# Performance work log

Measured on AMD Instinct MI355X. Metric: run time of the kernel, lower is better.

Reference implementation:

```python
import math
import jax, jax.numpy as jnp
import numpy as np

LOW_FREQ = 1
FACTOR = 1


def setup_inputs() -> dict:
    key = jax.random.key(0)
    x = jax.random.normal(key, (16, 4096, 256), dtype=jnp.float32)
    return {"x": x}


def reference(x):
    b, t, d = x.shape
    x_freq = jnp.fft.rfft(x, axis=1)  # (b, t//2+1, d) complex
    if t % 2 == 0:
        x_freq = x_freq[:, LOW_FREQ:-1]
        f = jnp.fft.rfftfreq(t)[LOW_FREQ:-1]
    else:
        x_freq = x_freq[:, LOW_FREQ:]
        f = jnp.fft.rfftfreq(t)[LOW_FREQ:]
    f = f.astype(jnp.float32)
    F = x_freq.shape[1]
    top_k = int(FACTOR * math.log(F))  # static (shape-derived)

    # top-k by magnitude along freq axis, independently per (b, d)
    xf_bdf = jnp.moveaxis(x_freq, 1, 2)              # (b, d, F)
    _, idx = jax.lax.top_k(jnp.abs(xf_bdf), top_k)   # (b, d, k) int32
    xf_sel = jnp.take_along_axis(xf_bdf, idx, axis=2)  # (b, d, k)
    xf_sel = jnp.moveaxis(xf_sel, 2, 1)              # (b, k, d)
    f_sel = jnp.moveaxis(f[idx], 2, 1)[:, :, None, :]  # (b, k, 1, d)

    # extrapolate: conj-pair frequencies, synthesize cosines, reduce over freq
    xf2 = jnp.concatenate([xf_sel, jnp.conj(xf_sel)], axis=1)  # (b, 2k, d)
    f2 = jnp.concatenate([f_sel, -f_sel], axis=1)              # (b, 2k, 1, d)
    tt = jnp.arange(t, dtype=jnp.float32)[None, None, :, None]  # (1,1,t,1)
    amp = (jnp.abs(xf2) * 2.0 / t)[:, :, None, :]   # (b, 2k, 1, d)
    phase = jnp.angle(xf2)[:, :, None, :]           # (b, 2k, 1, d)
    x_time = amp * jnp.cos(2.0 * math.pi * f2 * tt + phase)  # (b, 2k, t, d)
    return x_time.sum(axis=1)  # (b, t, d)
```

## Files before the change

kernel.cpp:

```cpp
#include <hip/hip_runtime.h>
#include <math.h>

#define T_LEN 4096
#define N2    2048
#define TOPK  7
#define NCH   256
#define R8F 0.70710678f

#define AD(a) ((a) + ((a) >> 3) + ((a) >> 8))

__global__ __launch_bounds__(256) void prep_kernel(
    const float* __restrict__ x, float* __restrict__ xt,
    double2* __restrict__ tw, float2* __restrict__ twf)
{
    if (blockIdx.x < 16) {
        int p = blockIdx.x * 256 + threadIdx.x;
        double th = -2.0 * 3.14159265358979323846 * (double)p / (double)T_LEN;
        double c = cos(th), s = sin(th);
        tw[p]  = make_double2(c, s);
        twf[p] = make_float2((float)c, (float)s);
        return;
    }
    __shared__ float tile[64][65];
    const int bid = blockIdx.x - 16;
    const int t0  = (bid & 63) * 64;
    const int c0  = ((bid >> 6) & 3) * 64;
    const int b   = bid >> 8;
    const int tx4 = (threadIdx.x & 15) * 4;
    const int ty  = threadIdx.x >> 4;

    const float* src = x + (size_t)b * T_LEN * NCH;
    for (int r = 0; r < 4; ++r) {
        int t = ty + r * 16;
        float4 v = *(const float4*)(src + (size_t)(t0 + t) * NCH + c0 + tx4);
        tile[t][tx4 + 0] = v.x; tile[t][tx4 + 1] = v.y;
        tile[t][tx4 + 2] = v.z; tile[t][tx4 + 3] = v.w;
    }
    __syncthreads();
    float* dst = xt + (size_t)b * NCH * T_LEN;
    for (int r = 0; r < 4; ++r) {
        int c = ty + r * 16;
        float4 v = make_float4(tile[tx4 + 0][c], tile[tx4 + 1][c],
                               tile[tx4 + 2][c], tile[tx4 + 3][c]);
        *(float4*)(dst + (size_t)(c0 + c) * T_LEN + t0 + tx4) = v;
    }
}

__device__ __forceinline__ void dft8_twf(float ar[8], float ai[8],
                                         int base, const float2* __restrict__ twf)
{
    float t0r=ar[0]+ar[4], t0i=ai[0]+ai[4], t4r=ar[0]-ar[4], t4i=ai[0]-ai[4];
    float t1r=ar[1]+ar[5], t1i=ai[1]+ai[5], t5r=ar[1]-ar[5], t5i=ai[1]-ai[5];
    float t2r=ar[2]+ar[6], t2i=ai[2]+ai[6], t6r=ar[2]-ar[6], t6i=ai[2]-ai[6];
    float t3r=ar[3]+ar[7], t3i=ai[3]+ai[7], t7r=ar[3]-ar[7], t7i=ai[3]-ai[7];
    float s0r=t0r+t2r, s0i=t0i+t2i, s2r=t0r-t2r, s2i=t0i-t2i;
    float s1r=t1r+t3r, s1i=t1i+t3i, s3r=t1r-t3r, s3i=t1i-t3i;
    ar[0]=s0r+s1r; ai[0]=s0i+s1i;
    ar[4]=s0r-s1r; ai[4]=s0i-s1i;
    ar[2]=s2r+s3i; ai[2]=s2i-s3r;
    ar[6]=s2r-s3i; ai[6]=s2i+s3r;
    float c1r=R8F*(t5r+t5i), c1i=R8F*(t5i-t5r);
    float c2r=t6i,           c2i=-t6r;
    float c3r=R8F*(t7i-t7r), c3i=-R8F*(t7r+t7i);
    float d0r=t4r+c2r, d0i=t4i+c2i, d1r=t4r-c2r, d1i=t4i-c2i;
    float d2r=c1r+c3r, d2i=c1i+c3i, d3r=c1r-c3r, d3i=c1i-c3i;
    ar[1]=d0r+d2r; ai[1]=d0i+d2i;
    ar[5]=d0r-d2r; ai[5]=d0i-d2i;
    ar[3]=d1r+d3i; ai[3]=d1i-d3r;
    ar[7]=d1r-d3i; ai[7]=d1i+d3r;
#pragma unroll
    for (int m = 1; m < 8; ++m) {
        float2 w = twf[(base * m) & 4095];
        float xr = ar[m], xi = ai[m];
        ar[m] = w.x * xr - w.y * xi;
        ai[m] = w.x * xi + w.y * xr;
    }
}

__device__ __forceinline__ unsigned long long packkey32(float mag, int k) {
    return ((unsigned long long)__float_as_uint(mag) << 32)
         | (unsigned long long)(2047 - k);
}

__global__ __launch_bounds__(256, 8) void fft_topk_kernel(
    const float* __restrict__ xt, const double2* __restrict__ tw,
    const float2* __restrict__ twf,
    int* __restrict__ k_out, float4* __restrict__ ab4)
{
    __shared__ float2 zz[AD(N2 - 1) + 3];
    __shared__ unsigned long long wavetop[4 * TOPK];
    __shared__ unsigned long long selkey[TOPK];

    const int tid = threadIdx.x;
    const int bc  = blockIdx.x;
    const float2* xcol2 = (const float2*)(xt + (size_t)bc * T_LEN);

    float ar[8], ai[8];
#pragma unroll
    for (int u = 0; u < 8; ++u) {
        float2 v = xcol2[tid + (u << 8)];
        ar[u] = v.x; ai[u] = v.y;
    }
    dft8_twf(ar, ai, 2 * tid, twf);
#pragma unroll
    for (int m = 0; m < 8; ++m)
        zz[AD((m << 8) + tid)] = make_float2(ar[m], ai[m]);
    __syncthreads();

    {
        const int g = tid >> 5, j2 = tid & 31, base = (g << 8) + j2;
#pragma unroll
        for (int u = 0; u < 8; ++u) {
            float2 v = zz[AD(base + (u << 5))];
            ar[u] = v.x; ai[u] = v.y;
        }
        dft8_twf(ar, ai, 16 * j2, twf);
#pragma unroll
        for (int m = 0; m < 8; ++m)
            zz[AD(base + (m << 5))] = make_float2(ar[m], ai[m]);
    }
    __syncthreads();

    {
        const int g3 = tid >> 2, j3 = tid & 3, base = (g3 << 5) + j3;
#pragma unroll
        for (int u = 0; u < 8; ++u) {
            float2 v = zz[AD(base + (u << 2))];
            ar[u] = v.x; ai[u] = v.y;
        }
        dft8_twf(ar, ai, 128 * j3, twf);
#pragma unroll
        for (int m = 0; m < 8; ++m)
            zz[AD(base + (m << 2))] = make_float2(ar[m], ai[m]);
    }
    __syncthreads();

#pragma unroll
    for (int q = 0; q < 2; ++q) {
        int h4 = ((q << 8) + tid) << 2;
#pragma unroll
        for (int r = 0; r < 4; ++r) {
            float2 v = zz[AD(h4 + r)];
            ar[q * 4 + r] = v.x; ai[q * 4 + r] = v.y;
        }
    }
    __syncthreads();
#pragma unroll
    for (int q = 0; q < 2; ++q) {
        float b0r = ar[q*4+0], b0i = ai[q*4+0], b1r = ar[q*4+1], b1i = ai[q*4+1];
        float b2r = ar[q*4+2], b2i = ai[q*4+2], b3r = ar[q*4+3], b3i = ai[q*4+3];
        float e0r = b0r + b2r, e0i = b0i + b2i, e1r = b0r - b2r, e1i = b0i - b2i;
        float e2r = b1r + b3r, e2i = b1i + b3i, e3r = b1r - b3r, e3i = b1i - b3i;
        int kbase = ((tid & 7) << 6) | (((tid >> 3) & 7) << 3) | (q << 2) | (tid >> 6);
        zz[AD(kbase)]        = make_float2(e0r + e2r, e0i + e2i);
        zz[AD(kbase + 1024)] = make_float2(e0r - e2r, e0i - e2i);
        zz[AD(kbase +  512)] = make_float2(e1r + e3i, e1i - e3r);
        zz[AD(kbase + 1536)] = make_float2(e1r - e3i, e1i + e3r);
    }
    __syncthreads();

    unsigned long long keys[8];
#pragma unroll
    for (int j = 0; j < 4; ++j) {
        int k  = 1 + tid + (j << 8);
        int kp = N2 - k;
        float2 yk = zz[AD(k)];
        float2 yp = zz[AD(kp)];
        float Ar = 0.5f * (yk.x + yp.x), Ai = 0.5f * (yk.y - yp.y);
        float Br = 0.5f * (yk.y + yp.y), Bi = -0.5f * (yk.x - yp.x);
        float2 t = twf[k];
        float Cr = t.x * Br - t.y * Bi;
        float Ci = t.x * Bi + t.y * Br;
        float m1 = (Ar + Cr) * (Ar + Cr) + (Ai + Ci) * (Ai + Ci);
        float m2 = (Ar - Cr) * (Ar - Cr) + (Ai - Ci) * (Ai - Ci);
        keys[2 * j]     = packkey32(m1, k);
        keys[2 * j + 1] = (kp != k) ? packkey32(m2, kp) : 0ULL;
    }

    const int wv = tid >> 6, ln = tid & 63;
    unsigned long long lb = 0ULL;
#pragma unroll
    for (int s = 0; s < 8; ++s) lb = (keys[s] > lb) ? keys[s] : lb;

    for (int it = 0; it < TOPK; ++it) {
        unsigned long long v = lb;
#pragma unroll
        for (int off = 32; off; off >>= 1) {
            unsigned long long o = __shfl_xor(v, off);
            if (o > v) v = o;
        }
        if (ln == 0) wavetop[wv * TOPK + it] = v;
#pragma unroll
        for (int s = 0; s < 8; ++s) keys[s] = (keys[s] == v) ? 0ULL : keys[s];
        lb = 0ULL;
#pragma unroll
        for (int s = 0; s < 8; ++s) lb = (keys[s] > lb) ? keys[s] : lb;
    }
    __syncthreads();

    if (tid < 32) {
        unsigned long long v = (tid < 4 * TOPK) ? wavetop[tid] : 0ULL;
        for (int it = 0; it < TOPK; ++it) {
            unsigned long long m = v;
#pragma unroll
            for (int off = 16; off; off >>= 1) {
                unsigned long long o = __shfl_xor(m, off);
                if (o > m) m = o;
            }
            if (tid == 0) selkey[it] = m;
            if (m == v) v = 0ULL;
        }
    }
    __syncthreads();

    if (tid < TOPK) {
        int k  = 2047 - (int)(selkey[tid] & 2047ULL);
        float2 ykf = zz[AD(k)];
        float2 ypf = zz[AD(N2 - k)];
        double ykx = (double)ykf.x, yky = (double)ykf.y;
        double ypx = (double)ypf.x, ypy = (double)ypf.y;
        double Ar = 0.5 * (ykx + ypx), Ai = 0.5 * (yky - ypy);
        double Br = 0.5 * (yky + ypy), Bi = -0.5 * (ykx - ypx);
        double2 t = tw[k];
        double Xr = Ar + t.x * Br - t.y * Bi;
        double Xi = Ai + t.x * Bi + t.y * Br;
        k_out[tid * 4096 + bc] = k;
        ab4[tid * 4096 + bc] = make_float4(
            (float)( 4.0 * Xr / (double)T_LEN),
            (float)(-4.0 * Xi / (double)T_LEN),
            (float)t.x, (float)(-t.y));
    }
}

__global__ __launch_bounds__(256) void recon_kernel(
    const int* __restrict__ k_in, const float4* __restrict__ ab4,
    float* __restrict__ out)
{
    __shared__ float tile[16][256];

    const int tid   = threadIdx.x;
    const int chunk = blockIdx.x & 127;
    const int b     = blockIdx.x >> 7;
    const int bc    = (b << 8) + tid;
    const int n0    = chunk << 5;

    const float c0 = 6.28318530717958647692f / 4096.0f;
    float aa[TOPK], bb[TOPK], zr[TOPK], zi[TOPK], wr[TOPK], wi[TOPK];
#pragma unroll
    for (int j = 0; j < TOPK; ++j) {
        int k    = k_in[j * 4096 + bc];
        float4 v = ab4[j * 4096 + bc];
        aa[j] = v.x; bb[j] = v.y; wr[j] = v.z; wi[j] = v.w;
        int m0 = (k * n0) & (T_LEN - 1);
        float ang = (float)m0 * c0;
        zr[j] = __cosf(ang);
        zi[j] = __sinf(ang);
    }

    float* obase = out + ((size_t)b * T_LEN + n0) * NCH;
    for (int r = 0; r < 2; ++r) {
#pragma unroll
        for (int i = 0; i < 16; ++i) {
            float acc = 0.f;
#pragma unroll
            for (int j = 0; j < TOPK; ++j) {
                acc += aa[j] * zr[j] + bb[j] * zi[j];
                float nzr = zr[j] * wr[j] - zi[j] * wi[j];
                zi[j] = zr[j] * wi[j] + zi[j] * wr[j];
                zr[j] = nzr;
            }
            tile[i][tid] = acc;
        }
        __syncthreads();
#pragma unroll
        for (int s = 0; s < 4; ++s) {
            int fid = tid + (s << 8);
            int ni  = fid >> 6;
            int c4  = (fid & 63) << 2;
            float4 v = make_float4(tile[ni][c4], tile[ni][c4 + 1],
                                   tile[ni][c4 + 2], tile[ni][c4 + 3]);
            *(float4*)(obase + (size_t)((r << 4) + ni) * NCH + c4) = v;
        }
        __syncthreads();
    }
}

extern "C" void kernel_launch(void* const* d_in, const int* in_sizes, int n_in,
                              void* d_out, int out_size, void* d_ws, size_t ws_size,
                              hipStream_t stream) {
    const float* x   = (const float*)d_in[0];
    float*       out = (float*)d_out;
    char*        ws  = (char*)d_ws;

    double2* tw    = (double2*)(ws);
    int*     k_ws  = (int*)   (ws + 65536);
    float4*  ab_ws = (float4*)(ws + 180224);
    float2*  twf   = (float2*)(ws + 638976);

    prep_kernel     <<<16 + 4096, 256, 0, stream>>>(x, out, tw, twf);
    fft_topk_kernel <<<4096, 256, 0, stream>>>(out, tw, twf, k_ws, ab_ws);
    recon_kernel    <<<2048, 256, 0, stream>>>(k_ws, ab_ws, out);
}
```

Measured before the change: 186.8 us.

## Compute FFT twiddles by powers, sort keys for top-k, halve recon blocks

Each radix-8 stage now loads one twiddle and builds its powers in registers instead of making seven table loads. Per-thread keys are sorted once with a sorting network, so each top-k round only shifts the list instead of rescanning all eight keys. The reconstruction kernel covers 64 time steps per block with half as many blocks, and re-seeds the recurrence with sincos every 16 steps to limit error build-up. The trade-offs are slightly lower twiddle accuracy from the power chain and fewer blocks in flight in recon.

```diff
diff --git a/kernel.cpp b/kernel.cpp
--- a/kernel.cpp
+++ b/kernel.cpp
@@ -46,8 +46,14 @@
     }
 }
 
-__device__ __forceinline__ void dft8_twf(float ar[8], float ai[8],
-                                         int base, const float2* __restrict__ twf)
+__device__ __forceinline__ void cmulf(float& xr, float& xi, float wrr, float wii) {
+    float r = wrr * xr - wii * xi;
+    xi = wrr * xi + wii * xr;
+    xr = r;
+}
+
+__device__ __forceinline__ void dft8_pw(float ar[8], float ai[8],
+                                        float w1r, float w1i)
 {
     float t0r=ar[0]+ar[4], t0i=ai[0]+ai[4], t4r=ar[0]-ar[4], t4i=ai[0]-ai[4];
     float t1r=ar[1]+ar[5], t1i=ai[1]+ai[5], t5r=ar[1]-ar[5], t5i=ai[1]-ai[5];
@@ -68,19 +74,29 @@
     ar[5]=d0r-d2r; ai[5]=d0i-d2i;
     ar[3]=d1r+d3i; ai[3]=d1i-d3r;
     ar[7]=d1r-d3i; ai[7]=d1i+d3r;
-#pragma unroll
-    for (int m = 1; m < 8; ++m) {
-        float2 w = twf[(base * m) & 4095];
-        float xr = ar[m], xi = ai[m];
-        ar[m] = w.x * xr - w.y * xi;
-        ai[m] = w.x * xi + w.y * xr;
-    }
+
+    float w2r = w1r*w1r - w1i*w1i, w2i = 2.0f*w1r*w1i;
+    float w3r = w2r*w1r - w2i*w1i, w3i = w2r*w1i + w2i*w1r;
+    float w4r = w2r*w2r - w2i*w2i, w4i = 2.0f*w2r*w2i;
+    float w5r = w3r*w2r - w3i*w2i, w5i = w3r*w2i + w3i*w2r;
+    float w6r = w3r*w3r - w3i*w3i, w6i = 2.0f*w3r*w3i;
+    float w7r = w4r*w3r - w4i*w3i, w7i = w4r*w3i + w4i*w3r;
+    cmulf(ar[1], ai[1], w1r, w1i);
+    cmulf(ar[2], ai[2], w2r, w2i);
+    cmulf(ar[3], ai[3], w3r, w3i);
+    cmulf(ar[4], ai[4], w4r, w4i);
+    cmulf(ar[5], ai[5], w5r, w5i);
+    cmulf(ar[6], ai[6], w6r, w6i);
+    cmulf(ar[7], ai[7], w7r, w7i);
 }
 
 __device__ __forceinline__ unsigned long long packkey32(float mag, int k) {
     return ((unsigned long long)__float_as_uint(mag) << 32)
          | (unsigned long long)(2047 - k);
 }
+
+#define CSWAP(i, j) { unsigned long long a_ = keys[i], b_ = keys[j]; \
+                      keys[i] = a_ > b_ ? a_ : b_; keys[j] = a_ > b_ ? b_ : a_; }
 
 __global__ __launch_bounds__(256, 8) void fft_topk_kernel(
     const float* __restrict__ xt, const double2* __restrict__ tw,
@@ -101,7 +117,10 @@
         float2 v = xcol2[tid + (u << 8)];
         ar[u] = v.x; ai[u] = v.y;
     }
-    dft8_twf(ar, ai, 2 * tid, twf);
+    {
+        float2 w1 = twf[2 * tid];
+        dft8_pw(ar, ai, w1.x, w1.y);
+    }
 #pragma unroll
     for (int m = 0; m < 8; ++m)
         zz[AD((m << 8) + tid)] = make_float2(ar[m], ai[m]);
@@ -114,7 +133,8 @@
             float2 v = zz[AD(base + (u << 5))];
             ar[u] = v.x; ai[u] = v.y;
         }
-        dft8_twf(ar, ai, 16 * j2, twf);
+        float2 w1 = twf[16 * j2];
+        dft8_pw(ar, ai, w1.x, w1.y);
 #pragma unroll
         for (int m = 0; m < 8; ++m)
             zz[AD(base + (m << 5))] = make_float2(ar[m], ai[m]);
@@ -128,7 +148,8 @@
             float2 v = zz[AD(base + (u << 2))];
             ar[u] = v.x; ai[u] = v.y;
         }
-        dft8_twf(ar, ai, 128 * j3, twf);
+        float2 w1 = twf[128 * j3];
+        dft8_pw(ar, ai, w1.x, w1.y);
 #pragma unroll
         for (int m = 0; m < 8; ++m)
             zz[AD(base + (m << 2))] = make_float2(ar[m], ai[m]);
@@ -177,10 +198,15 @@
         keys[2 * j + 1] = (kp != k) ? packkey32(m2, kp) : 0ULL;
     }
 
+    CSWAP(0,1) CSWAP(2,3) CSWAP(4,5) CSWAP(6,7)
+    CSWAP(0,2) CSWAP(1,3) CSWAP(4,6) CSWAP(5,7)
+    CSWAP(1,2) CSWAP(5,6)
+    CSWAP(0,4) CSWAP(1,5) CSWAP(2,6) CSWAP(3,7)
+    CSWAP(2,4) CSWAP(3,5)
+    CSWAP(1,2) CSWAP(3,4) CSWAP(5,6)
+
     const int wv = tid >> 6, ln = tid & 63;
-    unsigned long long lb = 0ULL;
-#pragma unroll
-    for (int s = 0; s < 8; ++s) lb = (keys[s] > lb) ? keys[s] : lb;
+    unsigned long long lb = keys[0];
 
     for (int it = 0; it < TOPK; ++it) {
         unsigned long long v = lb;
@@ -190,11 +216,11 @@
             if (o > v) v = o;
         }
         if (ln == 0) wavetop[wv * TOPK + it] = v;
-#pragma unroll
-        for (int s = 0; s < 8; ++s) keys[s] = (keys[s] == v) ? 0ULL : keys[s];
-        lb = 0ULL;
-#pragma unroll
-        for (int s = 0; s < 8; ++s) lb = (keys[s] > lb) ? keys[s] : lb;
+        if (v == lb && v) {
+            keys[0]=keys[1]; keys[1]=keys[2]; keys[2]=keys[3]; keys[3]=keys[4];
+            keys[4]=keys[5]; keys[5]=keys[6]; keys[6]=keys[7]; keys[7]=0ULL;
+            lb = keys[0];
+        }
     }
     __syncthreads();
 
@@ -239,26 +265,30 @@
     __shared__ float tile[16][256];
 
     const int tid   = threadIdx.x;
-    const int chunk = blockIdx.x & 127;
-    const int b     = blockIdx.x >> 7;
+    const int chunk = blockIdx.x & 63;
+    const int b     = blockIdx.x >> 6;
     const int bc    = (b << 8) + tid;
-    const int n0    = chunk << 5;
+    const int n0    = chunk << 6;
 
     const float c0 = 6.28318530717958647692f / 4096.0f;
+    int   kk[TOPK];
     float aa[TOPK], bb[TOPK], zr[TOPK], zi[TOPK], wr[TOPK], wi[TOPK];
 #pragma unroll
     for (int j = 0; j < TOPK; ++j) {
-        int k    = k_in[j * 4096 + bc];
+        kk[j] = k_in[j * 4096 + bc];
         float4 v = ab4[j * 4096 + bc];
         aa[j] = v.x; bb[j] = v.y; wr[j] = v.z; wi[j] = v.w;
-        int m0 = (k * n0) & (T_LEN - 1);
-        float ang = (float)m0 * c0;
-        zr[j] = __cosf(ang);
-        zi[j] = __sinf(ang);
     }
 
     float* obase = out + ((size_t)b * T_LEN + n0) * NCH;
-    for (int r = 0; r < 2; ++r) {
+    for (int sub = 0; sub < 4; ++sub) {
+        int ns = n0 + (sub << 4);
+#pragma unroll
+        for (int j = 0; j < TOPK; ++j) {
+            int m0 = (kk[j] * ns) & (T_LEN - 1);
+            float ang = (float)m0 * c0;
+            __sincosf(ang, &zi[j], &zr[j]);
+        }
 #pragma unroll
         for (int i = 0; i < 16; ++i) {
             float acc = 0.f;
@@ -279,7 +309,7 @@
             int c4  = (fid & 63) << 2;
             float4 v = make_float4(tile[ni][c4], tile[ni][c4 + 1],
                                    tile[ni][c4 + 2], tile[ni][c4 + 3]);
-            *(float4*)(obase + (size_t)((r << 4) + ni) * NCH + c4) = v;
+            *(float4*)(obase + (size_t)((sub << 4) + ni) * NCH + c4) = v;
         }
         __syncthreads();
     }
@@ -299,5 +329,5 @@
 
     prep_kernel     <<<16 + 4096, 256, 0, stream>>>(x, out, tw, twf);
     fft_topk_kernel <<<4096, 256, 0, stream>>>(out, tw, twf, k_ws, ab_ws);
-    recon_kernel    <<<2048, 256, 0, stream>>>(k_ws, ab_ws, out);
-}
+    recon_kernel    <<<1024, 256, 0, stream>>>(k_ws, ab_ws, out);
+}
```

Result: faster. 181.6 us (-2.8%).
